# Kernel tuning notes

Measured on AMD Instinct MI355X. Metric: run time of the kernel, lower is better.

Reference implementation:

```python
import jax, jax.numpy as jnp
import numpy as np

N_NODES = 50000
N_EDGES = 800000
F_IN = 128
HIDDEN = 256
N_CLASSES = 4


def setup_inputs() -> dict:
    key = jax.random.key(0)
    k1, k2, k3, k4 = jax.random.split(key, 4)
    x = jax.random.normal(k1, (N_NODES, F_IN), dtype=jnp.float32)
    edge_index = jax.random.randint(k2, (2, N_EDGES), 0, N_NODES, dtype=jnp.int64)
    # Glorot-style init for the two GCNConv linear layers (PyG GCNConv: W then bias)
    s1 = (6.0 / (F_IN + HIDDEN)) ** 0.5
    s2 = (6.0 / (HIDDEN + N_CLASSES)) ** 0.5
    W1 = jax.random.uniform(k3, (F_IN, HIDDEN), jnp.float32, -s1, s1)
    W2 = jax.random.uniform(k4, (HIDDEN, N_CLASSES), jnp.float32, -s2, s2)
    b1 = jnp.zeros((HIDDEN,), jnp.float32)
    b2 = jnp.zeros((N_CLASSES,), jnp.float32)
    return {"x": x, "edge_index": edge_index, "W1": W1, "b1": b1, "W2": W2, "b2": b2}


def _gcn_conv(x, W, b, src, dst, n_nodes):
    # PyG GCNConv: h = x @ W; add self-loops; symmetric D^{-1/2}(A+I)D^{-1/2} aggregation; + bias
    h = x @ W                                            # [N, out]
    deg = jnp.zeros((n_nodes,), h.dtype).at[dst].add(1.0) + 1.0  # +1 for self-loop
    dis = jax.lax.rsqrt(deg)                             # deg^{-1/2}
    norm = dis[src] * dis[dst]                           # [E]
    msg = norm[:, None] * h[src]                         # [E, out] per-edge messages
    agg = jax.ops.segment_sum(msg, dst, num_segments=n_nodes)
    agg = agg + (dis * dis)[:, None] * h                 # self-loop contribution
    return agg + b


def reference(x, edge_index, W1, b1, W2, b2):
    src, dst = edge_index[0], edge_index[1]
    h = _gcn_conv(x, W1, b1, src, dst, N_NODES)
    h = jax.nn.relu(h)
    # F.dropout with training=False (eval/inference reference) is identity
    out = _gcn_conv(h, W2, b2, src, dst, N_NODES)
    return out
```

## Files before the change

### kernel.cpp

```cpp
#include <hip/hip_runtime.h>

#define F_IN   128
#define HIDDEN 256
#define NCLS   4

#define BSH    7
#define BNODES 128
#define BCAP   3072
#define CHUNK  4096
#define NCAP   64

typedef __attribute__((ext_vector_type(8))) short short8;
typedef __attribute__((ext_vector_type(4))) float f32x4;

__device__ __forceinline__ unsigned short f2bf(float f) {
    unsigned int u = __float_as_uint(f);
    return (unsigned short)((u + 0x7fffu + ((u >> 16) & 1u)) >> 16);
}

__device__ __forceinline__ float bflo(unsigned int u) { return __uint_as_float(u << 16); }
__device__ __forceinline__ float bfhi(unsigned int u) { return __uint_as_float(u & 0xffff0000u); }


__global__ __launch_bounds__(256) void k_bin(const int* __restrict__ srcIdx,
                                             const int* __restrict__ dstIdx,
                                             int* __restrict__ cursor,
                                             unsigned int* __restrict__ inter,
                                             int E, int nbuk) {
    __shared__ int cntS[512], bA[512], bB[512], curS[512], eS[512], gS[512];
    __shared__ unsigned int stag[CHUNK];
    __shared__ unsigned short bb[CHUNK];
    int t = threadIdx.x;
    int e0 = blockIdx.x * CHUNK;
    int n = E - e0; if (n > CHUNK) n = CHUNK;

    cntS[t] = 0; cntS[t + 256] = 0;
    __syncthreads();
    for (int i = t; i < n; i += 256)
        atomicAdd(&cntS[dstIdx[e0 + i] >> BSH], 1);
    __syncthreads();

    int* pa = bA; int* pb = bB;
    bA[t] = cntS[t]; bA[t + 256] = cntS[t + 256];
    __syncthreads();
    for (int off = 1; off < 512; off <<= 1) {
        pb[t] = pa[t] + (t >= off ? pa[t - off] : 0);
        int p1 = t + 256;
        pb[p1] = pa[p1] + (p1 >= off ? pa[p1 - off] : 0);
        __syncthreads();
        int* tmp = pa; pa = pb; pb = tmp;
    }
    eS[t] = pa[t] - cntS[t];
    curS[t] = eS[t];
    int p1 = t + 256;
    eS[p1] = pa[p1] - cntS[p1];
    curS[p1] = eS[p1];
    __syncthreads();

    for (int i = t; i < nbuk; i += 256) {
        int c = cntS[i];
        gS[i] = (c > 0) ? atomicAdd(&cursor[i], c) : 0;
    }
    __syncthreads();

    for (int i = t; i < n; i += 256) {
        int d = dstIdx[e0 + i];
        int s = srcIdx[e0 + i];
        int b = d >> BSH;
        unsigned int w = ((unsigned int)(d & (BNODES - 1)) << 16) | (unsigned int)s;
        int off = atomicAdd(&curS[b], 1);
        stag[off] = w;
        bb[off] = (unsigned short)b;
    }
    __syncthreads();

    for (int i = t; i < n; i += 256) {
        int b = bb[i];
        inter[(size_t)b * BCAP + gS[b] + (i - eS[b])] = stag[i];
    }
}


__global__ __launch_bounds__(256) void k_bucket_build(const unsigned int* __restrict__ inter,
                                                      const int* __restrict__ cursor,
                                                      const float2* __restrict__ x2,
                                                      float* __restrict__ dis,
                                                      int* __restrict__ degPad,
                                                      unsigned int* __restrict__ xs,
                                                      unsigned short* __restrict__ csr16,
                                                      int N, int nbuk) {
    __shared__ int cntS[BNODES], curS[BNODES];
    __shared__ float disS[BNODES];
    __shared__ __align__(16) unsigned short csrS[BNODES * NCAP];
    int t = threadIdx.x;
    int b = blockIdx.x;
    int node0 = b << BSH;
    int nloc = N - node0; if (nloc > BNODES) nloc = BNODES;
    int cntb = cursor[b];
    const unsigned int* ip = inter + (size_t)b * BCAP;

    if (t < BNODES) { cntS[t] = 0; curS[t] = 0; }
    __syncthreads();
    for (int i = t; i < cntb; i += 256)
        atomicAdd(&cntS[ip[i] >> 16], 1);
    __syncthreads();

    if (t < nloc) {
        int c = cntS[t];
        float d = rsqrtf((float)c + 1.0f);
        dis[node0 + t] = d;
        disS[t] = d;
        degPad[node0 + t] = (c + 7) & ~7;
    }
    __syncthreads();

    for (int i = t; i < cntb; i += 256) {
        unsigned int w = ip[i];
        int nl = w >> 16;
        int off = atomicAdd(&curS[nl], 1);
        csrS[nl * NCAP + off] = (unsigned short)(w & 0xffffu);
    }
    __syncthreads();

    if (t < nloc) {
        unsigned short* a = &csrS[t * NCAP];
        int c = cntS[t];
        for (int i = 1; i < c; ++i) {
            unsigned short key = a[i];
            int j = i - 1;
            while (j >= 0 && a[j] > key) { a[j + 1] = a[j]; --j; }
            a[j + 1] = key;
        }
        int p = (c + 7) & ~7;
        for (int k = c; k < p; ++k) a[k] = (unsigned short)N;
    }
    __syncthreads();

    for (int g = t; g < nloc * (NCAP / 8); g += 256) {
        int nl = g >> 3;
        int sl = (g & 7) * 8;
        if (sl < ((cntS[nl] + 7) & ~7)) {
            *(uint4*)&csr16[((size_t)(node0 + nl)) * NCAP + sl] =
                *(const uint4*)&csrS[nl * NCAP + sl];
        }
    }

    for (int i = t; i < nloc * 64; i += 256) {
        int nl = i >> 6, l = i & 63;
        float d = disS[nl];
        float2 v = x2[((size_t)(node0 + nl)) * 64 + l];
        xs[((size_t)(node0 + nl)) * 64 + l] =
            (unsigned int)f2bf(d * v.x) | ((unsigned int)f2bf(d * v.y) << 16);
    }
    if (b == 0) {
        if (t < 64) xs[(size_t)N * 64 + t] = 0u;
        if (t == 64) dis[N] = 0.f;
    }
}


__global__ __launch_bounds__(256) void k_w1f_zero(const float* __restrict__ W1,
                                                  unsigned short* __restrict__ W1f,
                                                  int* __restrict__ cursor, int nbuk) {
    int t = blockIdx.x * 256 + threadIdx.x;
    if (t < nbuk) cursor[t] = 0;
    int lane = t & 63;
    int ks = (t >> 6) & 3;
    int ct = t >> 8;
    int n = ct * 16 + (lane & 15);
    int k0 = ks * 32 + (lane >> 4) * 8;
    unsigned int w[4];
#pragma unroll
    for (int p = 0; p < 4; ++p) {
        unsigned int lo = f2bf(W1[(k0 + 2 * p + 0) * HIDDEN + n]);
        unsigned int hi = f2bf(W1[(k0 + 2 * p + 1) * HIDDEN + n]);
        w[p] = lo | (hi << 16);
    }
    *(uint4*)(W1f + (size_t)t * 8) = make_uint4(w[0], w[1], w[2], w[3]);
}


__global__ __launch_bounds__(256) void k_pull_x(const unsigned short* __restrict__ csr16,
                                                const int* __restrict__ degPad,
                                                const float* __restrict__ dis,
                                                const unsigned int* __restrict__ xs,
                                                const float2* __restrict__ x2,
                                                unsigned int* __restrict__ aggB, int N) {
    int wave = threadIdx.x >> 6;
    int node = blockIdx.x * 4 + wave;
    int l = threadIdx.x & 63;
    if (node >= N) return;
    int dp = degPad[node];
    const unsigned short* cp = csr16 + (size_t)node * NCAP;
    float ax = 0.f, ay = 0.f;
    for (int e = 0; e < dp; e += 8) {
        uint4 iv = *(const uint4*)(cp + e);
        int s0 = iv.x & 0xffff, s1 = iv.x >> 16;
        int s2 = iv.y & 0xffff, s3 = iv.y >> 16;
        int s4 = iv.z & 0xffff, s5 = iv.z >> 16;
        int s6 = iv.w & 0xffff, s7 = iv.w >> 16;
        unsigned int u0 = xs[(size_t)s0 * 64 + l];
        unsigned int u1 = xs[(size_t)s1 * 64 + l];
        unsigned int u2 = xs[(size_t)s2 * 64 + l];
        unsigned int u3 = xs[(size_t)s3 * 64 + l];
        unsigned int u4 = xs[(size_t)s4 * 64 + l];
        unsigned int u5 = xs[(size_t)s5 * 64 + l];
        unsigned int u6 = xs[(size_t)s6 * 64 + l];
        unsigned int u7 = xs[(size_t)s7 * 64 + l];
        ax += bflo(u0) + bflo(u1) + bflo(u2) + bflo(u3) + bflo(u4) + bflo(u5) + bflo(u6) + bflo(u7);
        ay += bfhi(u0) + bfhi(u1) + bfhi(u2) + bfhi(u3) + bfhi(u4) + bfhi(u5) + bfhi(u6) + bfhi(u7);
    }
    float dd = dis[node];
    float sd = dd * dd;
    float2 xv = x2[(size_t)node * 64 + l];
    float ox = dd * ax + sd * xv.x;
    float oy = dd * ay + sd * xv.y;
    aggB[(size_t)node * 64 + l] = (unsigned int)f2bf(ox) | ((unsigned int)f2bf(oy) << 16);
}


__global__ __launch_bounds__(256) void k_gemm_mfma(const unsigned short* __restrict__ aggB,
                                                   const unsigned short* __restrict__ W1f,
                                                   const float* __restrict__ b1,
                                                   const float* __restrict__ W2,
                                                   float* __restrict__ Z, int N) {
    int wave = threadIdx.x >> 6;
    int lane = threadIdx.x & 63;
    int tile = blockIdx.x * 4 + wave;
    int row0 = tile * 16;
    if (row0 > N) return;
    int q = lane >> 4;
    int c16 = lane & 15;

    short8 a[4];
    const unsigned short* arow = aggB + (size_t)(row0 + c16) * F_IN;
#pragma unroll
    for (int ks = 0; ks < 4; ++ks)
        a[ks] = *(const short8*)(arow + ks * 32 + q * 8);

    float p[4][4] = {{0.f}};
#pragma unroll
    for (int ct = 0; ct < 16; ++ct) {
        f32x4 c = {0.f, 0.f, 0.f, 0.f};
#pragma unroll
        for (int ks = 0; ks < 4; ++ks) {
            short8 b = *(const short8*)(W1f + ((size_t)((ct * 4 + ks) * 64 + lane)) * 8);
            c = __builtin_amdgcn_mfma_f32_16x16x32_bf16(a[ks], b, c, 0, 0, 0);
        }
        int n = ct * 16 + c16;
        float bias = b1[n];
        float4 w2v = *(const float4*)(W2 + n * NCLS);
#pragma unroll
        for (int r = 0; r < 4; ++r) {
            float h = c[r] + bias;
            h = h > 0.f ? h : 0.f;
            p[r][0] += h * w2v.x;
            p[r][1] += h * w2v.y;
            p[r][2] += h * w2v.z;
            p[r][3] += h * w2v.w;
        }
    }
#pragma unroll
    for (int m = 1; m < 16; m <<= 1) {
#pragma unroll
        for (int r = 0; r < 4; ++r) {
#pragma unroll
            for (int j = 0; j < 4; ++j)
                p[r][j] += __shfl_xor(p[r][j], m);
        }
    }
    if (c16 == 0) {
#pragma unroll
        for (int r = 0; r < 4; ++r) {
            int row = row0 + q * 4 + r;
            if (row < N)
                *(float4*)(Z + (size_t)row * NCLS) = make_float4(p[r][0], p[r][1], p[r][2], p[r][3]);
            else if (row == N)
                *(float4*)(Z + (size_t)row * NCLS) = make_float4(0.f, 0.f, 0.f, 0.f);
        }
    }
}


__global__ __launch_bounds__(256) void k_pull_z(const unsigned short* __restrict__ csr16,
                                                const int* __restrict__ degPad,
                                                const float* __restrict__ dis,
                                                const float* __restrict__ Z,
                                                const float* __restrict__ b2,
                                                float* __restrict__ out, int N) {
    int t = blockIdx.x * blockDim.x + threadIdx.x;
    int node = t >> 2;
    int j = t & 3;
    if (node >= N) return;
    int dp = degPad[node];
    const unsigned short* cp = csr16 + (size_t)node * NCAP;
    float acc = 0.f;
    for (int e = 0; e < dp; e += 8) {
        uint4 iv = *(const uint4*)(cp + e);
        int s0 = iv.x & 0xffff, s1 = iv.x >> 16;
        int s2 = iv.y & 0xffff, s3 = iv.y >> 16;
        int s4 = iv.z & 0xffff, s5 = iv.z >> 16;
        int s6 = iv.w & 0xffff, s7 = iv.w >> 16;
        acc += dis[s0] * Z[(size_t)s0 * NCLS + j] + dis[s1] * Z[(size_t)s1 * NCLS + j]
             + dis[s2] * Z[(size_t)s2 * NCLS + j] + dis[s3] * Z[(size_t)s3 * NCLS + j]
             + dis[s4] * Z[(size_t)s4 * NCLS + j] + dis[s5] * Z[(size_t)s5 * NCLS + j]
             + dis[s6] * Z[(size_t)s6 * NCLS + j] + dis[s7] * Z[(size_t)s7 * NCLS + j];
    }
    float dd = dis[node];
    out[(size_t)node * NCLS + j] = dd * acc + dd * dd * Z[(size_t)node * NCLS + j] + b2[j];
}


extern "C" void kernel_launch(void* const* d_in, const int* in_sizes, int n_in,
                              void* d_out, int out_size, void* d_ws, size_t ws_size,
                              hipStream_t stream) {
    const float* x      = (const float*)d_in[0];
    const int*   ei     = (const int*)d_in[1];
    const float* W1     = (const float*)d_in[2];
    const float* b1     = (const float*)d_in[3];
    const float* W2     = (const float*)d_in[4];
    const float* b2     = (const float*)d_in[5];
    float* out          = (float*)d_out;

    const int N = in_sizes[0] / F_IN;
    const int E = in_sizes[1] / 2;
    const int* srcIdx = ei;
    const int* dstIdx = ei + E;

    const int nbuk = (N + BNODES - 1) >> BSH;

    unsigned short* aggB = (unsigned short*)d_ws;
    unsigned short* xsB  = aggB + (size_t)(N + 16) * F_IN;
    unsigned short* W1f  = xsB + (size_t)(N + 8) * F_IN;
    float* Z    = (float*)(W1f + 32768);
    float* dis  = Z + (size_t)(N + 4) * NCLS;
    int* degPad = (int*)(dis + N + 4);
    int* cursor = degPad + N;
    unsigned short* csr16 = (unsigned short*)(cursor + 512);
    unsigned int* inter = (unsigned int*)(csr16 + (size_t)N * NCAP);

    k_w1f_zero<<<16, 256, 0, stream>>>(W1, W1f, cursor, nbuk);
    k_bin<<<(E + CHUNK - 1) / CHUNK, 256, 0, stream>>>(srcIdx, dstIdx, cursor, inter, E, nbuk);
    k_bucket_build<<<nbuk, 256, 0, stream>>>(inter, cursor, (const float2*)x,
                                             dis, degPad, (unsigned int*)xsB, csr16, N, nbuk);
    k_pull_x<<<(N + 3) / 4, 256, 0, stream>>>(csr16, degPad, dis, (const unsigned int*)xsB,
                                              (const float2*)x, (unsigned int*)aggB, N);
    const int nTiles = N / 16 + 1;
    k_gemm_mfma<<<(nTiles + 3) / 4, 256, 0, stream>>>(aggB, W1f, b1, W2, Z, N);
    k_pull_z<<<(N * 4 + 255) / 256, 256, 0, stream>>>(csr16, degPad, dis, Z, b2, out, N);
}
```

Measured before the change: 206.6 us.

## Replace per-thread LDS insertion sort with wave-level bitonic sort kernel

The single-thread insertion sort of each node's neighbor list in LDS is removed from the bucket-build kernel, and unsorted neighbor lists are written straight to global memory. A new kernel then runs a 64-lane shuffle-based bitonic sort per node, one wave per node. This targets the serial, divergent insertion sort, which leaves most threads idle. In exchange it adds a kernel launch, scattered 2-byte global writes, and an extra global read and write of the CSR.

After: 180.8 us. 1.14x faster.

```diff
diff --git a/kernel.cpp b/kernel.cpp
--- a/kernel.cpp
+++ b/kernel.cpp
@@ -91,7 +91,6 @@
                                                       int N, int nbuk) {
     __shared__ int cntS[BNODES], curS[BNODES];
     __shared__ float disS[BNODES];
-    __shared__ __align__(16) unsigned short csrS[BNODES * NCAP];
     int t = threadIdx.x;
     int b = blockIdx.x;
     int node0 = b << BSH;
@@ -118,31 +117,12 @@
         unsigned int w = ip[i];
         int nl = w >> 16;
         int off = atomicAdd(&curS[nl], 1);
-        csrS[nl * NCAP + off] = (unsigned short)(w & 0xffffu);
-    }
-    __syncthreads();
-
+        csr16[((size_t)(node0 + nl)) * NCAP + off] = (unsigned short)(w & 0xffffu);
+    }
     if (t < nloc) {
-        unsigned short* a = &csrS[t * NCAP];
-        int c = cntS[t];
-        for (int i = 1; i < c; ++i) {
-            unsigned short key = a[i];
-            int j = i - 1;
-            while (j >= 0 && a[j] > key) { a[j + 1] = a[j]; --j; }
-            a[j + 1] = key;
-        }
-        int p = (c + 7) & ~7;
-        for (int k = c; k < p; ++k) a[k] = (unsigned short)N;
-    }
-    __syncthreads();
-
-    for (int g = t; g < nloc * (NCAP / 8); g += 256) {
-        int nl = g >> 3;
-        int sl = (g & 7) * 8;
-        if (sl < ((cntS[nl] + 7) & ~7)) {
-            *(uint4*)&csr16[((size_t)(node0 + nl)) * NCAP + sl] =
-                *(const uint4*)&csrS[nl * NCAP + sl];
-        }
+        int c = cntS[t], p = (c + 7) & ~7;
+        for (int k = c; k < p; ++k)
+            csr16[((size_t)(node0 + t)) * NCAP + k] = (unsigned short)N;
     }
 
     for (int i = t; i < nloc * 64; i += 256) {
@@ -156,6 +136,31 @@
         if (t < 64) xs[(size_t)N * 64 + t] = 0u;
         if (t == 64) dis[N] = 0.f;
     }
+}
+
+
+__global__ __launch_bounds__(256) void k_sort(unsigned short* __restrict__ csr16,
+                                              const int* __restrict__ degPad, int N) {
+    int wave = threadIdx.x >> 6;
+    int node = blockIdx.x * 4 + wave;
+    int l = threadIdx.x & 63;
+    if (node >= N) return;
+    int dp = degPad[node];
+    unsigned short* cp = csr16 + (size_t)node * NCAP;
+    int v = (l < dp) ? (int)cp[l] : 0xFFFF;
+#pragma unroll
+    for (int k = 2; k <= 64; k <<= 1) {
+#pragma unroll
+        for (int j = k >> 1; j > 0; j >>= 1) {
+            int p = __shfl_xor(v, j);
+            int mn = p < v ? p : v;
+            int mx = p < v ? v : p;
+            bool up = ((l & k) == 0);
+            bool lower = ((l & j) == 0);
+            v = (up == lower) ? mn : mx;
+        }
+    }
+    if (l < dp) cp[l] = (unsigned short)v;
 }
 
 
@@ -343,6 +348,7 @@
     k_bin<<<(E + CHUNK - 1) / CHUNK, 256, 0, stream>>>(srcIdx, dstIdx, cursor, inter, E, nbuk);
     k_bucket_build<<<nbuk, 256, 0, stream>>>(inter, cursor, (const float2*)x,
                                              dis, degPad, (unsigned int*)xsB, csr16, N, nbuk);
+    k_sort<<<(N + 3) / 4, 256, 0, stream>>>(csr16, degPad, N);
     k_pull_x<<<(N + 3) / 4, 256, 0, stream>>>(csr16, degPad, dis, (const unsigned int*)xsB,
                                               (const float2*)x, (unsigned int*)aggB, N);
     const int nTiles = N / 16 + 1;
```
